# Performance work log

Hardware: AMD Instinct MI355X
Metric: run time of the kernel (lower is better)

Reference implementation:

```python
import jax, jax.numpy as jnp
import numpy as np

N_NODES = 100000
N_REL = 16
N_BASES = 12
D_IN = 128   # initial_size
D_M1 = 128   # middle_size_1
D_M2 = 128   # middle_size_2
D_OUT3 = 512 - D_M2 - D_M1 - D_IN  # conv3 output = 128
N_EDGES = 1600000


def _param(key, shape, fan_in):
    return jax.random.normal(key, shape, dtype=jnp.float32) * (1.0 / np.sqrt(fan_in))


def setup_inputs() -> dict:
    key = jax.random.key(0)
    ks = jax.random.split(key, 16)
    inp = {
        'emb': _param(ks[0], (N_NODES, D_IN), D_IN),
        # conv1: 128 -> 128
        'comp1': _param(ks[1], (N_REL, N_BASES), N_BASES),
        'basis1': _param(ks[2], (N_BASES, D_IN, D_M1), D_IN),
        'root1': _param(ks[3], (D_IN, D_M1), D_IN),
        'bias1': jnp.zeros((D_M1,), jnp.float32),
        # conv2: 128 -> 128
        'comp2': _param(ks[4], (N_REL, N_BASES), N_BASES),
        'basis2': _param(ks[5], (N_BASES, D_M1, D_M2), D_M1),
        'root2': _param(ks[6], (D_M1, D_M2), D_M1),
        'bias2': jnp.zeros((D_M2,), jnp.float32),
        # conv3: 128 -> 128
        'comp3': _param(ks[7], (N_REL, N_BASES), N_BASES),
        'basis3': _param(ks[8], (N_BASES, D_M2, D_OUT3), D_M2),
        'root3': _param(ks[9], (D_M2, D_OUT3), D_M2),
        'bias3': jnp.zeros((D_OUT3,), jnp.float32),
        # graph structure
        'src': jax.random.randint(ks[10], (N_EDGES,), 0, N_NODES, dtype=jnp.int32),
        'tgt': jax.random.randint(ks[11], (N_EDGES,), 0, N_NODES, dtype=jnp.int32),
        'edge_type': jax.random.randint(ks[12], (N_EDGES,), 0, N_REL, dtype=jnp.int32),
    }
    return inp


def _rgcn_conv(x, comp, basis, root, bias, src, tgt, etype):
    """PyG RGCNConv with basis decomposition and per-(target,relation) mean aggr."""
    # basis-decomposed relation weights: [R, d_in, d_out]
    W = jnp.einsum('rb,bio->rio', comp, basis)
    d_in = x.shape[1]
    x_src = x[src]  # gather [E, d_in]
    # bucket-sum messages per (target node, relation): [N, R, d_in]
    S = jnp.zeros((N_NODES, N_REL, d_in), x.dtype).at[tgt, etype].add(x_src)
    cnt = jnp.zeros((N_NODES, N_REL), x.dtype).at[tgt, etype].add(1.0)
    mean = S / jnp.maximum(cnt, 1.0)[:, :, None]
    # transform per relation and sum over relations, plus root/self loop
    out = jnp.einsum('nrd,rdo->no', mean, W) + x @ root + bias
    return out


def reference(emb, comp1, basis1, root1, bias1, comp2, basis2, root2, bias2,
              comp3, basis3, root3, bias3, src, tgt, edge_type):
    x1 = jax.nn.relu(_rgcn_conv(emb, comp1, basis1, root1, bias1, src, tgt, edge_type))
    x2 = jax.nn.relu(_rgcn_conv(x1, comp2, basis2, root2, bias2, src, tgt, edge_type))
    x3 = jax.nn.relu(_rgcn_conv(x2, comp3, basis3, root3, bias3, src, tgt, edge_type))
    # dropout in eval mode = identity
    return jnp.concatenate((x3, x2, x1, emb), axis=1)
```

## Files before the change

kernel.cpp:

```cpp
#include <hip/hip_runtime.h>
#include <hip/hip_bf16.h>

#define NNODES 100000
#define NRELS  16
#define NEDGES 1600000
#define NBLKS  782
#define NKEYS  (NBLKS * 16)
#define GRID_MFMA 512

typedef unsigned short u16;
typedef unsigned int   u32;
typedef __attribute__((ext_vector_type(8))) short short8;
typedef __attribute__((ext_vector_type(4))) float f32x4;

#define WS_INVCNT   0
#define WS_OFFS     6400000
#define WS_CUR      6450064
#define WS_EMETA    6500112
#define WS_WTHI     19300112
#define WS_WTLO     19857168
#define WS_CTR      20414224
#define WS_END      20414240

#define MFMA16(a, b, c) __builtin_amdgcn_mfma_f32_16x16x32_bf16((a), (b), (c), 0, 0, 0)

__device__ __forceinline__ u16 bf16_rne(float v) {
    u32 u = __float_as_uint(v);
    u32 r = (u + 0x7FFFu + ((u >> 16) & 1u)) >> 16;
    return (u16)r;
}

__global__ void hist_kernel(const int* __restrict__ tgt, const int* __restrict__ et,
                            float* __restrict__ cnt, int* __restrict__ keyCnt) {
    int e = blockIdx.x * 256 + threadIdx.x;
    if (e >= NEDGES) return;
    int t = tgt[e], r = et[e];
    atomicAdd(&cnt[t * 16 + r], 1.0f);
    atomicAdd(&keyCnt[(t >> 7) * 16 + r], 1);
}

__global__ void scan_kernel(int* __restrict__ cur, int* __restrict__ offs) {
    __shared__ int part[256];
    int t = threadIdx.x;
    int lo = t * 49, hi = min(lo + 49, NKEYS);
    int s = 0;
    for (int i = lo; i < hi; ++i) s += cur[i];
    part[t] = s;
    __syncthreads();
    if (t == 0) {
        int run = 0;
        for (int i = 0; i < 256; ++i) { int v = part[i]; part[i] = run; run += v; }
        offs[NKEYS] = run;
    }
    __syncthreads();
    int run = part[t];
    for (int i = lo; i < hi; ++i) {
        int c = cur[i];
        offs[i] = run; cur[i] = run; run += c;
    }
}

__global__ void invcnt_kernel(float* __restrict__ cnt) {
    int i = blockIdx.x * 256 + threadIdx.x;
    if (i < NNODES * 16) cnt[i] = 1.0f / fmaxf(cnt[i], 1.0f);
}

__global__ void scatter_edges(const int* __restrict__ src, const int* __restrict__ tgt,
                              const int* __restrict__ et, const float* __restrict__ invcnt,
                              int* __restrict__ cur, int2* __restrict__ eMeta) {
    int e = blockIdx.x * 256 + threadIdx.x;
    if (e >= NEDGES) return;
    int t = tgt[e], r = et[e];
    int key = (t >> 7) * 16 + r;
    int pos = atomicAdd(&cur[key], 1);
    int2 m;
    m.x = src[e] | ((t & 127) << 20);
    m.y = __float_as_int(invcnt[t * 16 + r]);
    eMeta[pos] = m;
}

__global__ void wprep_kernel(const float* __restrict__ comp, const float* __restrict__ basis,
                             const float* __restrict__ root,
                             u16* __restrict__ Wthi, u16* __restrict__ Wtlo) {
    int t = blockIdx.x * 256 + threadIdx.x;
    if (t >= 17 * 128 * 32) return;
    int k4 = (t & 31) * 4, col = (t >> 5) & 127, rel = t >> 12;
    float v[4];
    if (rel < 16) {
        v[0] = v[1] = v[2] = v[3] = 0.f;
        #pragma unroll
        for (int b = 0; b < 12; ++b) {
            float c = comp[rel * 12 + b];
            #pragma unroll
            for (int kk = 0; kk < 4; ++kk)
                v[kk] += c * basis[b * 16384 + (k4 + kk) * 128 + col];
        }
    } else {
        #pragma unroll
        for (int kk = 0; kk < 4; ++kk) v[kk] = root[(k4 + kk) * 128 + col];
    }
    ushort4 h, l;
    u16* hp = (u16*)&h; u16* lp = (u16*)&l;
    #pragma unroll
    for (int kk = 0; kk < 4; ++kk) {
        hp[kk] = bf16_rne(v[kk]);
        lp[kk] = bf16_rne(v[kk] - __uint_as_float((u32)hp[kk] << 16));
    }
    size_t o = (size_t)rel * 16384 + col * 128 + k4;
    *reinterpret_cast<ushort4*>(Wthi + o) = h;
    *reinterpret_cast<ushort4*>(Wtlo + o) = l;
}

__global__ __launch_bounds__(256, 2) void layer_mfma(
    const float* __restrict__ xp, int xstride,
    const u16* __restrict__ Wthi, const u16* __restrict__ Wtlo,
    const float* __restrict__ bias,
    const int2* __restrict__ eMeta, const int* __restrict__ offs,
    int* __restrict__ jobCtr,
    float* __restrict__ out, int colOff)
{
    __shared__ float accS[128 * 132];
    __shared__ int sJb;
    const int tid = threadIdx.x;
    const int w  = tid >> 6;
    const int l  = tid & 63;
    const int g  = l >> 4;
    const int ln = l & 15;
    const int colb = w * 32;

    short8 Bh[2][4], Bl[2][4];

    while (true) {
        if (tid == 0) sJb = atomicAdd(jobCtr, 1);
        __syncthreads();
        const int b = sJb;
        if (b >= NBLKS) break;
        const int node0 = b * 128;
        const int nIn = min(128, NNODES - node0);

        for (int i = tid; i < 128 * 128; i += 256)
            accS[(i >> 7) * 132 + (i & 127)] = bias[i & 127];
        __syncthreads();

        for (int rel = 0; rel <= 16; ++rel) {
            int s0, s1;
            if (rel < 16) { s0 = offs[b * 16 + rel]; s1 = offs[b * 16 + rel + 1]; }
            else          { s0 = 0; s1 = nIn; }
            if (s0 >= s1) continue;

            {
                const u16* ph = Wthi + (size_t)rel * 16384 + (colb + ln) * 128 + g * 8;
                const u16* pl = Wtlo + (size_t)rel * 16384 + (colb + ln) * 128 + g * 8;
                #pragma unroll
                for (int nf = 0; nf < 2; ++nf)
                    #pragma unroll
                    for (int kc = 0; kc < 4; ++kc) {
                        Bh[nf][kc] = *(const short8*)(ph + nf * 2048 + kc * 32);
                        Bl[nf][kc] = *(const short8*)(pl + nf * 2048 + kc * 32);
                    }
            }

            auto loadT = [&](int t0, float4* raw, int* tg, float* sc) {
                int aSrc;
                if (rel < 16) {
                    aSrc = eMeta[min(t0 + ln, s1 - 1)].x & 0xFFFFF;
                    #pragma unroll
                    for (int j = 0; j < 4; ++j) {
                        int ei = t0 + 4 * g + j;
                        int2 mj = eMeta[min(ei, s1 - 1)];
                        tg[j] = (mj.x >> 20) & 127;
                        sc[j] = (ei < s1) ? __int_as_float(mj.y) : 0.f;
                    }
                } else {
                    aSrc = node0 + min(t0 + ln, s1 - 1);
                    #pragma unroll
                    for (int j = 0; j < 4; ++j) {
                        int ei = t0 + 4 * g + j;
                        tg[j] = min(ei, s1 - 1);
                        sc[j] = (ei < s1) ? 1.f : 0.f;
                    }
                }
                const float* pa = xp + (size_t)aSrc * xstride + g * 8;
                #pragma unroll
                for (int kc = 0; kc < 4; ++kc) {
                    raw[2 * kc]     = *reinterpret_cast<const float4*>(pa + kc * 32);
                    raw[2 * kc + 1] = *reinterpret_cast<const float4*>(pa + kc * 32 + 4);
                }
            };
            auto computeT = [&](const float4* raw, const int* tg, const float* sc) {
                f32x4 a0 = {0.f, 0.f, 0.f, 0.f}, a1 = {0.f, 0.f, 0.f, 0.f};
                #pragma unroll
                for (int kc = 0; kc < 4; ++kc) {
                    short8 ah, al;
                    const float* f = reinterpret_cast<const float*>(&raw[2 * kc]);
                    #pragma unroll
                    for (int j = 0; j < 8; ++j) {
                        u32 u = __float_as_uint(f[j]);
                        u16 h = (u16)(u >> 16);
                        float d = f[j] - __uint_as_float((u32)h << 16);
                        ah[j] = (short)h;
                        al[j] = (short)bf16_rne(d);
                    }
                    a0 = MFMA16(al, Bh[0][kc], a0);
                    a0 = MFMA16(ah, Bl[0][kc], a0);
                    a0 = MFMA16(ah, Bh[0][kc], a0);
                    a1 = MFMA16(al, Bh[1][kc], a1);
                    a1 = MFMA16(ah, Bl[1][kc], a1);
                    a1 = MFMA16(ah, Bh[1][kc], a1);
                }
                #pragma unroll
                for (int j = 0; j < 4; ++j) {
                    if (sc[j] != 0.f) {
                        float* p = &accS[tg[j] * 132 + colb + ln];
                        atomicAdd(p,      a0[j] * sc[j]);
                        atomicAdd(p + 16, a1[j] * sc[j]);
                    }
                }
            };

            float4 rawA[8], rawB[8];
            int tgA[4], tgB[4]; float scA[4], scB[4];
            loadT(s0, rawA, tgA, scA);
            for (int t0 = s0; t0 < s1; t0 += 32) {
                const int t1 = t0 + 16;
                if (t1 < s1) loadT(t1, rawB, tgB, scB);
                computeT(rawA, tgA, scA);
                if (t1 < s1) {
                    if (t1 + 16 < s1) loadT(t1 + 16, rawA, tgA, scA);
                    computeT(rawB, tgB, scB);
                }
            }
        }
        __syncthreads();
        for (int q = tid; q < nIn * 32; q += 256) {
            int r = q >> 5, c = (q & 31) * 4;
            float4 v = *reinterpret_cast<const float4*>(&accS[r * 132 + c]);
            v.x = fmaxf(v.x, 0.f); v.y = fmaxf(v.y, 0.f);
            v.z = fmaxf(v.z, 0.f); v.w = fmaxf(v.w, 0.f);
            *reinterpret_cast<float4*>(out + (size_t)(node0 + r) * 512 + colOff + c) = v;
        }
        __syncthreads();
    }
}

__global__ void emb_copy(const float* __restrict__ emb, float* __restrict__ out) {
    int q = blockIdx.x * 256 + threadIdx.x;
    int n = q >> 5, c = (q & 31) * 4;
    float4 v = *reinterpret_cast<const float4*>(emb + (size_t)n * 128 + c);
    *reinterpret_cast<float4*>(out + (size_t)n * 512 + 384 + c) = v;
}

extern "C" void kernel_launch(void* const* d_in, const int* in_sizes, int n_in,
                              void* d_out, int out_size, void* d_ws, size_t ws_size,
                              hipStream_t stream) {
    const float* emb = (const float*)d_in[0];
    const float* comp[3]  = {(const float*)d_in[1], (const float*)d_in[5], (const float*)d_in[9]};
    const float* basis[3] = {(const float*)d_in[2], (const float*)d_in[6], (const float*)d_in[10]};
    const float* root[3]  = {(const float*)d_in[3], (const float*)d_in[7], (const float*)d_in[11]};
    const float* bias[3]  = {(const float*)d_in[4], (const float*)d_in[8], (const float*)d_in[12]};
    const int* src = (const int*)d_in[13];
    const int* tgt = (const int*)d_in[14];
    const int* et  = (const int*)d_in[15];
    float* out = (float*)d_out;

    char* ws = (char*)d_ws;
    float* invcnt = (float*)(ws + WS_INVCNT);
    int*   offs   = (int*)(ws + WS_OFFS);
    int*   cur    = (int*)(ws + WS_CUR);
    int2*  eMeta  = (int2*)(ws + WS_EMETA);
    u16*   Wthi   = (u16*)(ws + WS_WTHI);
    u16*   Wtlo   = (u16*)(ws + WS_WTLO);
    int*   jobCtr = (int*)(ws + WS_CTR);
    if (ws_size < (size_t)WS_END) return;

    hipMemsetAsync(invcnt, 0, 6400000, stream);
    hipMemsetAsync(cur, 0, NKEYS * 4, stream);
    hipMemsetAsync(jobCtr, 0, 16, stream);
    hist_kernel<<<6250, 256, 0, stream>>>(tgt, et, invcnt, cur);
    scan_kernel<<<1, 256, 0, stream>>>(cur, offs);
    invcnt_kernel<<<6250, 256, 0, stream>>>(invcnt);
    scatter_edges<<<6250, 256, 0, stream>>>(src, tgt, et, invcnt, cur, eMeta);

    const float* xin[3] = {emb, out + 256, out + 128};
    const int    xs[3]  = {128, 512, 512};
    const int    colOff[3] = {256, 128, 0};

    for (int lyr = 0; lyr < 3; ++lyr) {
        wprep_kernel<<<272, 256, 0, stream>>>(comp[lyr], basis[lyr], root[lyr], Wthi, Wtlo);
        layer_mfma<<<GRID_MFMA, 256, 0, stream>>>(xin[lyr], xs[lyr], Wthi, Wtlo, bias[lyr],
                                                  eMeta, offs, jobCtr + lyr, out, colOff[lyr]);
    }
    emb_copy<<<12500, 256, 0, stream>>>(emb, out);
}
```

Measured before the change: 4.879 ms.

## Split K across waves and triple-buffer edge gathers in RGCN MFMA layer

Result: slower. 9.009 ms (+84.6%).

```diff
diff --git a/kernel.cpp b/kernel.cpp
--- a/kernel.cpp
+++ b/kernel.cpp
@@ -122,13 +122,72 @@
     __shared__ float accS[128 * 132];
     __shared__ int sJb;
     const int tid = threadIdx.x;
-    const int w  = tid >> 6;
-    const int l  = tid & 63;
-    const int g  = l >> 4;
-    const int ln = l & 15;
-    const int colb = w * 32;
-
-    short8 Bh[2][4], Bl[2][4];
+    const int w   = tid >> 6;
+    const int kh  = w >> 1;
+    const int ch  = w & 1;
+    const int l   = tid & 63;
+    const int g   = l >> 4;
+    const int ln  = l & 15;
+    const int cbase = ch * 64 + ln;
+    const int kfl   = kh * 64 + g * 8;
+
+    short8 Bh[8], Bl[8];
+
+#define LOADM(T, SRC, T0, T1, T2, T3, S0, S1_, S2, S3) do {                     \
+        if (rel < 16) {                                                         \
+            SRC = eMeta[min((T) + ln, s1 - 1)].x & 0xFFFFF;                     \
+            int2 m0_ = eMeta[min((T) + 4 * g + 0, s1 - 1)];                     \
+            int2 m1_ = eMeta[min((T) + 4 * g + 1, s1 - 1)];                     \
+            int2 m2_ = eMeta[min((T) + 4 * g + 2, s1 - 1)];                     \
+            int2 m3_ = eMeta[min((T) + 4 * g + 3, s1 - 1)];                     \
+            T0 = (m0_.x >> 20) & 127; S0  = ((T)+4*g+0 < s1) ? __int_as_float(m0_.y) : 0.f; \
+            T1 = (m1_.x >> 20) & 127; S1_ = ((T)+4*g+1 < s1) ? __int_as_float(m1_.y) : 0.f; \
+            T2 = (m2_.x >> 20) & 127; S2  = ((T)+4*g+2 < s1) ? __int_as_float(m2_.y) : 0.f; \
+            T3 = (m3_.x >> 20) & 127; S3  = ((T)+4*g+3 < s1) ? __int_as_float(m3_.y) : 0.f; \
+        } else {                                                                \
+            SRC = node0 + min((T) + ln, s1 - 1);                                \
+            T0 = min((T)+4*g+0, s1-1); S0  = ((T)+4*g+0 < s1) ? 1.f : 0.f;      \
+            T1 = min((T)+4*g+1, s1-1); S1_ = ((T)+4*g+1 < s1) ? 1.f : 0.f;      \
+            T2 = min((T)+4*g+2, s1-1); S2  = ((T)+4*g+2 < s1) ? 1.f : 0.f;      \
+            T3 = min((T)+4*g+3, s1-1); S3  = ((T)+4*g+3 < s1) ? 1.f : 0.f;      \
+        } } while (0)
+
+#define LOADX(SRC, X0, X1, X2, X3) do {                                         \
+        const float* pa_ = xp + (size_t)(SRC) * xstride + kfl;                  \
+        X0 = *reinterpret_cast<const float4*>(pa_);                             \
+        X1 = *reinterpret_cast<const float4*>(pa_ + 4);                         \
+        X2 = *reinterpret_cast<const float4*>(pa_ + 32);                        \
+        X3 = *reinterpret_cast<const float4*>(pa_ + 36); } while (0)
+
+#define SPLIT8(F0, F1, AH, AL) do {                                             \
+        float ft_[8] = {F0.x, F0.y, F0.z, F0.w, F1.x, F1.y, F1.z, F1.w};        \
+        _Pragma("unroll")                                                       \
+        for (int jj = 0; jj < 8; ++jj) {                                        \
+            u32 u_ = __float_as_uint(ft_[jj]);                                  \
+            u16 h_ = (u16)(u_ >> 16);                                           \
+            float d_ = ft_[jj] - __uint_as_float((u32)h_ << 16);                \
+            AH[jj] = (short)h_; AL[jj] = (short)bf16_rne(d_);                   \
+        } } while (0)
+
+#define COMPUTE(X0, X1, X2, X3, T0, T1, T2, T3, S0, S1_, S2, S3) do {           \
+        short8 ah0_, al0_, ah1_, al1_;                                          \
+        SPLIT8(X0, X1, ah0_, al0_);                                             \
+        SPLIT8(X2, X3, ah1_, al1_);                                             \
+        _Pragma("unroll")                                                       \
+        for (int cf = 0; cf < 4; ++cf) {                                        \
+            f32x4 a_ = {0.f, 0.f, 0.f, 0.f};                                    \
+            a_ = MFMA16(al0_, Bh[cf * 2 + 0], a_);                              \
+            a_ = MFMA16(ah0_, Bl[cf * 2 + 0], a_);                              \
+            a_ = MFMA16(ah0_, Bh[cf * 2 + 0], a_);                              \
+            a_ = MFMA16(al1_, Bh[cf * 2 + 1], a_);                              \
+            a_ = MFMA16(ah1_, Bl[cf * 2 + 1], a_);                              \
+            a_ = MFMA16(ah1_, Bh[cf * 2 + 1], a_);                              \
+            float* pc_ = &accS[cbase + cf * 16];                                \
+            if (S0  != 0.f) atomicAdd(pc_ + T0 * 132, a_[0] * S0);              \
+            if (S1_ != 0.f) atomicAdd(pc_ + T1 * 132, a_[1] * S1_);             \
+            if (S2  != 0.f) atomicAdd(pc_ + T2 * 132, a_[2] * S2);              \
+            if (S3  != 0.f) atomicAdd(pc_ + T3 * 132, a_[3] * S3);              \
+        } } while (0)
 
     while (true) {
         if (tid == 0) sJb = atomicAdd(jobCtr, 1);
@@ -149,86 +208,41 @@
             if (s0 >= s1) continue;
 
             {
-                const u16* ph = Wthi + (size_t)rel * 16384 + (colb + ln) * 128 + g * 8;
-                const u16* pl = Wtlo + (size_t)rel * 16384 + (colb + ln) * 128 + g * 8;
+                const u16* pbh = Wthi + (size_t)rel * 16384 + (size_t)(ch * 64 + ln) * 128 + kh * 64 + g * 8;
+                const u16* pbl = Wtlo + (size_t)rel * 16384 + (size_t)(ch * 64 + ln) * 128 + kh * 64 + g * 8;
                 #pragma unroll
-                for (int nf = 0; nf < 2; ++nf)
+                for (int cf = 0; cf < 4; ++cf)
                     #pragma unroll
-                    for (int kc = 0; kc < 4; ++kc) {
-                        Bh[nf][kc] = *(const short8*)(ph + nf * 2048 + kc * 32);
-                        Bl[nf][kc] = *(const short8*)(pl + nf * 2048 + kc * 32);
+                    for (int kc = 0; kc < 2; ++kc) {
+                        Bh[cf * 2 + kc] = *reinterpret_cast<const short8*>(pbh + cf * 2048 + kc * 32);
+                        Bl[cf * 2 + kc] = *reinterpret_cast<const short8*>(pbl + cf * 2048 + kc * 32);
                     }
             }
 
-            auto loadT = [&](int t0, float4* raw, int* tg, float* sc) {
-                int aSrc;
-                if (rel < 16) {
-                    aSrc = eMeta[min(t0 + ln, s1 - 1)].x & 0xFFFFF;
-                    #pragma unroll
-                    for (int j = 0; j < 4; ++j) {
-                        int ei = t0 + 4 * g + j;
-                        int2 mj = eMeta[min(ei, s1 - 1)];
-                        tg[j] = (mj.x >> 20) & 127;
-                        sc[j] = (ei < s1) ? __int_as_float(mj.y) : 0.f;
-                    }
-                } else {
-                    aSrc = node0 + min(t0 + ln, s1 - 1);
-                    #pragma unroll
-                    for (int j = 0; j < 4; ++j) {
-                        int ei = t0 + 4 * g + j;
-                        tg[j] = min(ei, s1 - 1);
-                        sc[j] = (ei < s1) ? 1.f : 0.f;
-                    }
-                }
-                const float* pa = xp + (size_t)aSrc * xstride + g * 8;
-                #pragma unroll
-                for (int kc = 0; kc < 4; ++kc) {
-                    raw[2 * kc]     = *reinterpret_cast<const float4*>(pa + kc * 32);
-                    raw[2 * kc + 1] = *reinterpret_cast<const float4*>(pa + kc * 32 + 4);
-                }
-            };
-            auto computeT = [&](const float4* raw, const int* tg, const float* sc) {
-                f32x4 a0 = {0.f, 0.f, 0.f, 0.f}, a1 = {0.f, 0.f, 0.f, 0.f};
-                #pragma unroll
-                for (int kc = 0; kc < 4; ++kc) {
-                    short8 ah, al;
-                    const float* f = reinterpret_cast<const float*>(&raw[2 * kc]);
-                    #pragma unroll
-                    for (int j = 0; j < 8; ++j) {
-                        u32 u = __float_as_uint(f[j]);
-                        u16 h = (u16)(u >> 16);
-                        float d = f[j] - __uint_as_float((u32)h << 16);
-                        ah[j] = (short)h;
-                        al[j] = (short)bf16_rne(d);
-                    }
-                    a0 = MFMA16(al, Bh[0][kc], a0);
-                    a0 = MFMA16(ah, Bl[0][kc], a0);
-                    a0 = MFMA16(ah, Bh[0][kc], a0);
-                    a1 = MFMA16(al, Bh[1][kc], a1);
-                    a1 = MFMA16(ah, Bl[1][kc], a1);
-                    a1 = MFMA16(ah, Bh[1][kc], a1);
-                }
-                #pragma unroll
-                for (int j = 0; j < 4; ++j) {
-                    if (sc[j] != 0.f) {
-                        float* p = &accS[tg[j] * 132 + colb + ln];
-                        atomicAdd(p,      a0[j] * sc[j]);
-                        atomicAdd(p + 16, a1[j] * sc[j]);
-                    }
-                }
-            };
-
-            float4 rawA[8], rawB[8];
-            int tgA[4], tgB[4]; float scA[4], scB[4];
-            loadT(s0, rawA, tgA, scA);
-            for (int t0 = s0; t0 < s1; t0 += 32) {
-                const int t1 = t0 + 16;
-                if (t1 < s1) loadT(t1, rawB, tgB, scB);
-                computeT(rawA, tgA, scA);
-                if (t1 < s1) {
-                    if (t1 + 16 < s1) loadT(t1 + 16, rawA, tgA, scA);
-                    computeT(rawB, tgB, scB);
-                }
+            int   srcA, tA0, tA1, tA2, tA3;  float sA0, sA1, sA2, sA3;
+            int   srcB, tB0, tB1, tB2, tB3;  float sB0, sB1, sB2, sB3;
+            int   srcC, tC0, tC1, tC2, tC3;  float sC0, sC1, sC2, sC3;
+            float4 xA0, xA1, xA2, xA3, xB0, xB1, xB2, xB3, xC0, xC1, xC2, xC3;
+
+            int t = s0;
+            LOADM(t, srcA, tA0, tA1, tA2, tA3, sA0, sA1, sA2, sA3);
+            LOADX(srcA, xA0, xA1, xA2, xA3);
+            LOADM(t + 16, srcB, tB0, tB1, tB2, tB3, sB0, sB1, sB2, sB3);
+            for (;;) {
+                if (t + 16 < s1) LOADX(srcB, xB0, xB1, xB2, xB3);
+                LOADM(t + 32, srcC, tC0, tC1, tC2, tC3, sC0, sC1, sC2, sC3);
+                COMPUTE(xA0, xA1, xA2, xA3, tA0, tA1, tA2, tA3, sA0, sA1, sA2, sA3);
+                t += 16; if (t >= s1) break;
+
+                if (t + 16 < s1) LOADX(srcC, xC0, xC1, xC2, xC3);
+                LOADM(t + 32, srcA, tA0, tA1, tA2, tA3, sA0, sA1, sA2, sA3);
+                COMPUTE(xB0, xB1, xB2, xB3, tB0, tB1, tB2, tB3, sB0, sB1, sB2, sB3);
+                t += 16; if (t >= s1) break;
+
+                if (t + 16 < s1) LOADX(srcA, xA0, xA1, xA2, xA3);
+                LOADM(t + 32, srcB, tB0, tB1, tB2, tB3, sB0, sB1, sB2, sB3);
+                COMPUTE(xC0, xC1, xC2, xC3, tC0, tC1, tC2, tC3, sC0, sC1, sC2, sC3);
+                t += 16; if (t >= s1) break;
             }
         }
         __syncthreads();
@@ -241,6 +255,10 @@
         }
         __syncthreads();
     }
+#undef LOADM
+#undef LOADX
+#undef SPLIT8
+#undef COMPUTE
 }
 
 __global__ void emb_copy(const float* __restrict__ emb, float* __restrict__ out) {
```
